# Kernel optimization log

Hardware: AMD Instinct MI355X
Metric: run time of the kernel (lower is better)

## Reference

```python
import jax, jax.numpy as jnp
import numpy as np

DIM = 512
NUM_HEADS = 8
HEAD_DIM = DIM // NUM_HEADS
EPS = 1e-12  # F.normalize eps


def _l2norm(x):
    # F.normalize(x, dim=-1): x / max(||x||, eps)
    n = jnp.sqrt(jnp.sum(x * x, axis=-1, keepdims=True))
    return x / jnp.maximum(n, EPS)


def setup_inputs() -> dict:
    key = jax.random.key(0)
    ks = jax.random.split(key, 5)
    B, T, D = 4, 2048, DIM
    z = jax.random.normal(ks[0], (B, T, D), dtype=jnp.float32)
    t = jnp.zeros((1,), dtype=jnp.float32)  # unused ODE time
    omega = jax.random.normal(ks[1], (1, 1, D), dtype=jnp.float32) * 0.1
    # nn.Linear default init scale ~ U(-1/sqrt(fan_in), 1/sqrt(fan_in))
    s = 1.0 / np.sqrt(D)
    W_qk = jax.random.uniform(ks[2], (2 * D, D), jnp.float32, -s, s)
    W_out = jax.random.uniform(ks[3], (D, D), jnp.float32, -s, s)
    b_out = jax.random.uniform(ks[4], (D,), jnp.float32, -s, s)
    return {"t": t, "z": z, "omega": omega, "W_qk": W_qk, "W_out": W_out, "b_out": b_out}


def reference(t, z, omega, W_qk, W_out, b_out):
    B, T, D = z.shape
    H, hd = NUM_HEADS, HEAD_DIM
    qk = z @ W_qk.T                      # [B,T,2D]
    q, k = qk[..., :D], qk[..., D:]
    q = _l2norm(q.reshape(B, T, H, hd))  # [B,T,H,hd]
    k = _l2norm(k.reshape(B, T, H, hd))
    # coupling: [B,H,T,T]
    coupling = jnp.einsum("bqhd,bkhd->bhqk", q, k)
    interaction = jnp.sin(coupling)
    force = jnp.einsum("bhqk,bkhd->bqhd", interaction, k).reshape(B, T, D)
    return omega + force @ W_out.T + b_out
```

## Files before the change

kernel.cpp:

```cpp
#include <hip/hip_runtime.h>
#include <hip/hip_bf16.h>

typedef unsigned short u16;
typedef _Float16 f16;
typedef __attribute__((ext_vector_type(8))) _Float16 f16x8;
typedef __attribute__((ext_vector_type(2))) __fp16 h16x2;
typedef __attribute__((ext_vector_type(8))) short short8;
typedef __attribute__((ext_vector_type(4))) float f32x4;

#define B_ 4
#define T_ 2048
#define D_ 512
#define H_ 8
#define M_ (B_*T_)
#define INV2PI 0.15915494309189535f

__device__ f16 g_qb[M_*D_];
__device__ f16 g_kb[M_*D_];
__device__ f16 g_kTp[(size_t)B_*H_*64*T_];
__device__ f16 g_fA[(size_t)M_*D_];
__device__ f16 g_fB[(size_t)M_*D_];

__device__ inline float sin2pi(float x) {
#if __has_builtin(__builtin_amdgcn_sinf)
  return __builtin_amdgcn_sinf(x);
#else
  return __sinf(x * 6.283185307179586f);
#endif
}

__device__ inline void gload16(const void* g, void* l) {
  __builtin_amdgcn_global_load_lds(
      (const __attribute__((address_space(1))) unsigned int*)g,
      (__attribute__((address_space(3))) unsigned int*)l, 16, 0, 0);
}

__device__ inline f16x8 cvt8h(f32x4 a, f32x4 b) {
  union { h16x2 h[4]; f16x8 v; } u;
  u.h[0] = __builtin_amdgcn_cvt_pkrtz(a[0], a[1]);
  u.h[1] = __builtin_amdgcn_cvt_pkrtz(a[2], a[3]);
  u.h[2] = __builtin_amdgcn_cvt_pkrtz(b[0], b[1]);
  u.h[3] = __builtin_amdgcn_cvt_pkrtz(b[2], b[3]);
  return u.v;
}

__device__ inline int perm5(int p) {
  int lg = p >> 3, e = p & 7;
  return (e < 4) ? lg*4 + e : 16 + lg*4 + (e & 3);
}

template<int MODE>
__global__ __launch_bounds__(256, 2)
void gemm_bt(float* __restrict__ Cout, const float* __restrict__ add1,
             const float* __restrict__ add2, const float* __restrict__ Afp,
             const float* __restrict__ Bfp) {
  constexpr int K = 512;
  constexpr int N = (MODE == 0) ? 1024 : 512;
  __shared__ f16 As[128*72];
  __shared__ f16 Bs[128*72];
  const int m0 = blockIdx.x*128, n0 = blockIdx.y*128;
  const int t = threadIdx.x;
  const int w = t>>6, l = t&63;
  const int wr = (w>>1)*64, wc = (w&1)*64;
  const int lg = l>>4, li = l&15;
  const int srow = t>>3, scol = (t&7)*8;

  f32x4 acc[4][4] = {};

  for (int k0 = 0; k0 < K; k0 += 64) {
#pragma unroll
    for (int p = 0; p < 4; ++p) {
      int r = srow + p*32;
      {
        f32x4 b0 = *(const f32x4*)&Bfp[(size_t)(n0+r)*K + k0 + scol];
        f32x4 b1 = *(const f32x4*)&Bfp[(size_t)(n0+r)*K + k0 + scol + 4];
        *(f16x8*)&Bs[r*72 + scol] = cvt8h(b0, b1);
      }
      if (MODE == 0) {
        f32x4 a0 = *(const f32x4*)&Afp[(size_t)(m0+r)*K + k0 + scol];
        f32x4 a1 = *(const f32x4*)&Afp[(size_t)(m0+r)*K + k0 + scol + 4];
        *(f16x8*)&As[r*72 + scol] = cvt8h(a0, a1);
      } else {
        f16x8 a = *(const f16x8*)&g_fA[(size_t)(m0+r)*K + k0 + scol];
        f16x8 c = *(const f16x8*)&g_fB[(size_t)(m0+r)*K + k0 + scol];
        *(f16x8*)&As[r*72 + scol] = a + c;
      }
    }
    __syncthreads();
#pragma unroll
    for (int ks = 0; ks < 2; ++ks) {
      f16x8 af[4], bf[4];
#pragma unroll
      for (int i = 0; i < 4; ++i)
        af[i] = *(const f16x8*)&As[(wr + i*16 + li)*72 + ks*32 + lg*8];
#pragma unroll
      for (int j = 0; j < 4; ++j)
        bf[j] = *(const f16x8*)&Bs[(wc + j*16 + li)*72 + ks*32 + lg*8];
#pragma unroll
      for (int i = 0; i < 4; ++i)
#pragma unroll
        for (int j = 0; j < 4; ++j)
          acc[i][j] = __builtin_amdgcn_mfma_f32_16x16x32_f16(af[i], bf[j], acc[i][j], 0, 0, 0);
    }
    __syncthreads();
  }

  if (MODE == 0) {
    const bool isq = (n0 < 512);
    f16* dst = isq ? g_qb : g_kb;
    const float qs = isq ? INV2PI : 1.0f;
    const int nb = (isq ? n0 : n0 - 512) + wc;
#pragma unroll
    for (int i = 0; i < 4; ++i) {
#pragma unroll
      for (int r = 0; r < 4; ++r) {
        float s = 0.f;
#pragma unroll
        for (int j = 0; j < 4; ++j) s += acc[i][j][r]*acc[i][j][r];
#pragma unroll
        for (int off = 1; off < 16; off <<= 1) s += __shfl_xor(s, off);
        float sc = qs / fmaxf(sqrtf(s), 1e-12f);
        int row = m0 + wr + i*16 + lg*4 + r;
#pragma unroll
        for (int j = 0; j < 4; ++j)
          dst[(size_t)row*D_ + nb + j*16 + li] = (f16)(acc[i][j][r]*sc);
      }
    }
  } else {
#pragma unroll
    for (int i = 0; i < 4; ++i) {
#pragma unroll
      for (int j = 0; j < 4; ++j) {
        int col = n0 + wc + j*16 + li;
        float badd = add1[col] + add2[col];
#pragma unroll
        for (int r = 0; r < 4; ++r) {
          int row = m0 + wr + i*16 + lg*4 + r;
          Cout[(size_t)row*N + col] = acc[i][j][r] + badd;
        }
      }
    }
  }
}

__global__ void transpose_k_kernel() {
  __shared__ u16 tile[64*72];
  const int t0 = blockIdx.x*64, bh = blockIdx.y;
  const int b = bh>>3, h = bh&7;
  const int t = threadIdx.x;
  const u16* kb = (const u16*)g_kb;
  u16* kT = (u16*)g_kTp;
  {
    int r = t>>2, cs = (t&3)*16;
    const u16* src = kb + (size_t)(b*T_ + t0 + r)*D_ + h*64 + cs;
    *(short8*)&tile[r*72 + cs]     = *(const short8*)(src);
    *(short8*)&tile[r*72 + cs + 8] = *(const short8*)(src + 8);
  }
  __syncthreads();
  {
    int d = t>>2, ts = (t&3)*16;
    short8 o0, o1;
#pragma unroll
    for (int j = 0; j < 8; ++j) {
      int p0 = ts + j, p1 = ts + 8 + j;
      int s0 = (p0 & ~31) | perm5(p0 & 31);
      int s1 = (p1 & ~31) | perm5(p1 & 31);
      o0[j] = (short)tile[s0*72 + d];
      o1[j] = (short)tile[s1*72 + d];
    }
    u16* dst = kT + ((size_t)bh*64 + d)*T_ + t0 + ts;
    *(short8*)(dst)     = o0;
    *(short8*)(dst + 8) = o1;
  }
}

__global__ __launch_bounds__(256, 2)
void kuramoto_attn_kernel() {
  __shared__ f16 Ks[2][128*64];
  __shared__ f16 KTs[2][64*128];
  const int wg  = blockIdx.x;
  const int wgp = (wg & 7)*64 + (wg >> 3);
  const int bh = wgp >> 4, qt = (wgp & 15) >> 1, kh = wgp & 1;
  const int b = bh >> 3, h = bh & 7;
  const int t = threadIdx.x;
  const int w = t>>6, l = t&63;
  const int lg = l>>4, li = l&15;

  f16x8 bq[2][4];
#pragma unroll
  for (int ks = 0; ks < 2; ++ks)
#pragma unroll
    for (int j = 0; j < 4; ++j)
      bq[ks][j] = *(const f16x8*)&g_qb[(size_t)(b*T_ + qt*256 + w*64 + j*16 + li)*D_
                                       + h*64 + ks*32 + lg*8];

  const f16* kbase = g_kb  + (size_t)b*T_*D_ + h*64;
  const f16* tbase = g_kTp + (size_t)bh*64*T_;
  const int kt0 = kh*8;

#define STAGE(BUFI, KT) do {                                                   \
  _Pragma("unroll") for (int p = 0; p < 4; ++p) {                              \
    int idx = (w*4+p)*64 + l;                                                  \
    int rK = idx >> 3, sK = idx & 7;                                           \
    gload16(&kbase[(size_t)((KT)*128 + rK)*D_ + ((sK ^ (rK & 7))<<3)],         \
            &Ks[BUFI][(w*4+p)*512]);                                           \
    int rT = idx >> 4, sT = idx & 15;                                          \
    gload16(&tbase[(size_t)rT*T_ + (KT)*128 + ((sT ^ (rT & 15))<<3)],          \
            &KTs[BUFI][(w*4+p)*512]);                                          \
  } } while(0)

  f32x4 acc_o[4][4] = {};

  STAGE(0, kt0);
  __syncthreads();

#define QK_STEP(KKP, S) do {                                                   \
  _Pragma("unroll") for (int ks = 0; ks < 2; ++ks) {                           \
    f16x8 af0 = *(const f16x8*)&Ks[buf][((2*(KKP)  )*16 + li)*64               \
                                        + (((ks*4+lg) ^ (li&7))<<3)];          \
    f16x8 af1 = *(const f16x8*)&Ks[buf][((2*(KKP)+1)*16 + li)*64               \
                                        + (((ks*4+lg) ^ (li&7))<<3)];          \
    __builtin_amdgcn_s_setprio(1);                                             \
    _Pragma("unroll") for (int j = 0; j < 4; ++j) {                            \
      S[0][j] = __builtin_amdgcn_mfma_f32_16x16x32_f16(af0, bq[ks][j], S[0][j], 0,0,0); \
      S[1][j] = __builtin_amdgcn_mfma_f32_16x16x32_f16(af1, bq[ks][j], S[1][j], 0,0,0); \
    }                                                                          \
    __builtin_amdgcn_s_setprio(0); } } while(0)

#define SINPV_STEP(KKP, S) do {                                                \
  f16x8 apv[4];                                                                \
  _Pragma("unroll") for (int j = 0; j < 4; ++j) {                              \
    union { h16x2 h[4]; f16x8 v; } cv;                                         \
    cv.h[0] = __builtin_amdgcn_cvt_pkrtz(sin2pi(S[0][j][0]), sin2pi(S[0][j][1])); \
    cv.h[1] = __builtin_amdgcn_cvt_pkrtz(sin2pi(S[0][j][2]), sin2pi(S[0][j][3])); \
    cv.h[2] = __builtin_amdgcn_cvt_pkrtz(sin2pi(S[1][j][0]), sin2pi(S[1][j][1])); \
    cv.h[3] = __builtin_amdgcn_cvt_pkrtz(sin2pi(S[1][j][2]), sin2pi(S[1][j][3])); \
    apv[j] = cv.v; }                                                           \
  _Pragma("unroll") for (int di = 0; di < 4; ++di) {                           \
    f16x8 bv = *(const f16x8*)&KTs[buf][(di*16 + li)*128                       \
                                        + ((((KKP)*4+lg) ^ li)<<3)];           \
    __builtin_amdgcn_s_setprio(1);                                             \
    _Pragma("unroll") for (int j = 0; j < 4; ++j)                              \
      acc_o[j][di] = __builtin_amdgcn_mfma_f32_16x16x32_f16(apv[j], bv, acc_o[j][di], 0,0,0); \
    __builtin_amdgcn_s_setprio(0);                                             \
  } } while(0)

#pragma unroll 2
  for (int ii = 0; ii < 8; ++ii) {
    const int buf = ii & 1;
    if (ii < 7) STAGE(buf^1, kt0 + ii + 1);

    f32x4 sA[2][4] = {};
    f32x4 sB[2][4] = {};
    QK_STEP(0, sA);
    QK_STEP(1, sB);  SINPV_STEP(0, sA);
#pragma unroll
    for (int z = 0; z < 2; ++z)
#pragma unroll
      for (int j = 0; j < 4; ++j) sA[z][j] = (f32x4)(0.f);
    QK_STEP(2, sA);  SINPV_STEP(1, sB);
#pragma unroll
    for (int z = 0; z < 2; ++z)
#pragma unroll
      for (int j = 0; j < 4; ++j) sB[z][j] = (f32x4)(0.f);
    QK_STEP(3, sB);  SINPV_STEP(2, sA);
                     SINPV_STEP(3, sB);

    __syncthreads();
  }
#undef QK_STEP
#undef SINPV_STEP
#undef STAGE

  f16* F = kh ? g_fB : g_fA;
#pragma unroll
  for (int j = 0; j < 4; ++j)
#pragma unroll
    for (int di = 0; di < 4; ++di)
#pragma unroll
      for (int r = 0; r < 4; ++r) {
        int row = b*T_ + qt*256 + w*64 + j*16 + lg*4 + r;
        int col = h*64 + di*16 + li;
        F[(size_t)row*D_ + col] = (f16)acc_o[j][di][r];
      }
}

extern "C" void kernel_launch(void* const* d_in, const int* in_sizes, int n_in,
                              void* d_out, int out_size, void* d_ws, size_t ws_size,
                              hipStream_t stream) {
  const float* z     = (const float*)d_in[1];
  const float* omega = (const float*)d_in[2];
  const float* Wqk   = (const float*)d_in[3];
  const float* Wout  = (const float*)d_in[4];
  const float* bout  = (const float*)d_in[5];
  float* out = (float*)d_out;

  gemm_bt<0><<<dim3(M_/128, 1024/128), 256, 0, stream>>>(nullptr, nullptr, nullptr, z, Wqk);
  transpose_k_kernel<<<dim3(T_/64, B_*H_), 256, 0, stream>>>();
  kuramoto_attn_kernel<<<512, 256, 0, stream>>>();
  gemm_bt<1><<<dim3(M_/128, 512/128), 256, 0, stream>>>(out, omega, bout, nullptr, Wout);
}
```

Baseline: 153.1 us.

## Fuse K transpose into QK projection epilogue and drop setprio hints

The QK projection GEMM epilogue now writes the permuted, transposed K layout directly for K tiles, which removes the separate transpose kernel launch and its extra read/write pass over K. The s_setprio calls around the MFMA blocks in the attention kernel are also removed. The fused writes are 8-byte scattered stores along strided rows, so they may coalesce less well than the old transpose kernel's stores. Removing setprio changes how waves are scheduled during the attention loop.

Result: faster. 149.2 us (-2.6%).

```diff
diff --git a/kernel.cpp b/kernel.cpp
--- a/kernel.cpp
+++ b/kernel.cpp
@@ -4,6 +4,7 @@
 typedef unsigned short u16;
 typedef _Float16 f16;
 typedef __attribute__((ext_vector_type(8))) _Float16 f16x8;
+typedef __attribute__((ext_vector_type(4))) _Float16 f16x4;
 typedef __attribute__((ext_vector_type(2))) __fp16 h16x2;
 typedef __attribute__((ext_vector_type(8))) short short8;
 typedef __attribute__((ext_vector_type(4))) float f32x4;
@@ -42,11 +43,6 @@
   u.h[2] = __builtin_amdgcn_cvt_pkrtz(b[0], b[1]);
   u.h[3] = __builtin_amdgcn_cvt_pkrtz(b[2], b[3]);
   return u.v;
-}
-
-__device__ inline int perm5(int p) {
-  int lg = p >> 3, e = p & 7;
-  return (e < 4) ? lg*4 + e : 16 + lg*4 + (e & 3);
 }
 
 template<int MODE>
@@ -110,6 +106,7 @@
     f16* dst = isq ? g_qb : g_kb;
     const float qs = isq ? INV2PI : 1.0f;
     const int nb = (isq ? n0 : n0 - 512) + wc;
+    f16 hv[4][4][4];
 #pragma unroll
     for (int i = 0; i < 4; ++i) {
 #pragma unroll
@@ -122,8 +119,29 @@
         float sc = qs / fmaxf(sqrtf(s), 1e-12f);
         int row = m0 + wr + i*16 + lg*4 + r;
 #pragma unroll
-        for (int j = 0; j < 4; ++j)
-          dst[(size_t)row*D_ + nb + j*16 + li] = (f16)(acc[i][j][r]*sc);
+        for (int j = 0; j < 4; ++j) {
+          f16 v = (f16)(acc[i][j][r]*sc);
+          hv[i][j][r] = v;
+          dst[(size_t)row*D_ + nb + j*16 + li] = v;
+        }
+      }
+    }
+    if (!isq) {
+      const int hh  = nb >> 6;
+      const int bh2 = (m0 >> 11)*H_ + hh;
+      const int t0b = (m0 & (T_-1)) + wr;
+#pragma unroll
+      for (int i = 0; i < 4; ++i) {
+        int tloc = t0b + i*16 + lg*4;
+        int g5 = tloc & ~31, k5 = tloc & 31;
+        int p5 = (k5 < 16) ? ((k5>>2)*8) : (((k5-16)>>2)*8 + 4);
+        int tpos = g5 + p5;
+#pragma unroll
+        for (int j = 0; j < 4; ++j) {
+          f16x4 v4;
+          v4[0]=hv[i][j][0]; v4[1]=hv[i][j][1]; v4[2]=hv[i][j][2]; v4[3]=hv[i][j][3];
+          *(f16x4*)&g_kTp[((size_t)bh2*64 + j*16 + li)*T_ + tpos] = v4;
+        }
       }
     }
   } else {
@@ -140,37 +158,6 @@
         }
       }
     }
-  }
-}
-
-__global__ void transpose_k_kernel() {
-  __shared__ u16 tile[64*72];
-  const int t0 = blockIdx.x*64, bh = blockIdx.y;
-  const int b = bh>>3, h = bh&7;
-  const int t = threadIdx.x;
-  const u16* kb = (const u16*)g_kb;
-  u16* kT = (u16*)g_kTp;
-  {
-    int r = t>>2, cs = (t&3)*16;
-    const u16* src = kb + (size_t)(b*T_ + t0 + r)*D_ + h*64 + cs;
-    *(short8*)&tile[r*72 + cs]     = *(const short8*)(src);
-    *(short8*)&tile[r*72 + cs + 8] = *(const short8*)(src + 8);
-  }
-  __syncthreads();
-  {
-    int d = t>>2, ts = (t&3)*16;
-    short8 o0, o1;
-#pragma unroll
-    for (int j = 0; j < 8; ++j) {
-      int p0 = ts + j, p1 = ts + 8 + j;
-      int s0 = (p0 & ~31) | perm5(p0 & 31);
-      int s1 = (p1 & ~31) | perm5(p1 & 31);
-      o0[j] = (short)tile[s0*72 + d];
-      o1[j] = (short)tile[s1*72 + d];
-    }
-    u16* dst = kT + ((size_t)bh*64 + d)*T_ + t0 + ts;
-    *(short8*)(dst)     = o0;
-    *(short8*)(dst + 8) = o1;
   }
 }
 
@@ -220,12 +207,10 @@
                                         + (((ks*4+lg) ^ (li&7))<<3)];          \
     f16x8 af1 = *(const f16x8*)&Ks[buf][((2*(KKP)+1)*16 + li)*64               \
                                         + (((ks*4+lg) ^ (li&7))<<3)];          \
-    __builtin_amdgcn_s_setprio(1);                                             \
     _Pragma("unroll") for (int j = 0; j < 4; ++j) {                            \
       S[0][j] = __builtin_amdgcn_mfma_f32_16x16x32_f16(af0, bq[ks][j], S[0][j], 0,0,0); \
       S[1][j] = __builtin_amdgcn_mfma_f32_16x16x32_f16(af1, bq[ks][j], S[1][j], 0,0,0); \
-    }                                                                          \
-    __builtin_amdgcn_s_setprio(0); } } while(0)
+    } } } while(0)
 
 #define SINPV_STEP(KKP, S) do {                                                \
   f16x8 apv[4];                                                                \
@@ -239,10 +224,8 @@
   _Pragma("unroll") for (int di = 0; di < 4; ++di) {                           \
     f16x8 bv = *(const f16x8*)&KTs[buf][(di*16 + li)*128                       \
                                         + ((((KKP)*4+lg) ^ li)<<3)];           \
-    __builtin_amdgcn_s_setprio(1);                                             \
     _Pragma("unroll") for (int j = 0; j < 4; ++j)                              \
       acc_o[j][di] = __builtin_amdgcn_mfma_f32_16x16x32_f16(apv[j], bv, acc_o[j][di], 0,0,0); \
-    __builtin_amdgcn_s_setprio(0);                                             \
   } } while(0)
 
 #pragma unroll 2
@@ -296,7 +279,6 @@
   float* out = (float*)d_out;
 
   gemm_bt<0><<<dim3(M_/128, 1024/128), 256, 0, stream>>>(nullptr, nullptr, nullptr, z, Wqk);
-  transpose_k_kernel<<<dim3(T_/64, B_*H_), 256, 0, stream>>>();
   kuramoto_attn_kernel<<<512, 256, 0, stream>>>();
   gemm_bt<1><<<dim3(M_/128, 512/128), 256, 0, stream>>>(out, omega, bout, nullptr, Wout);
 }
```
